# Optimization experiments

Measured on AMD Instinct MI355X. Metric: run time of the kernel, lower is better.

The kernel has to match this reference:

```python
import jax, jax.numpy as jnp
import numpy as np

HM = 256  # output_hm_shape


def _peak_grid(heatmap):
    # max_num_peaks=1 NMS -> global argmax per (b, joint) channel
    B, J, H, W = heatmap.shape
    idx = jnp.argmax(heatmap.reshape(B, J, H * W), axis=-1)
    y = (idx // W).astype(jnp.float32)
    x = (idx % W).astype(jnp.float32)
    ny = (H - 1) / 2.0
    nx = (W - 1) / 2.0
    # normalized (gx, gy) in [-1, 1], note (row,col) -> (x,y) flip as in source
    return jnp.stack([(x - nx) / nx, (y - ny) / ny], axis=-1)  # [B, J, 2]


def _bilinear_sample(feat, grid):
    # feat: [B, C, H, W], grid: [B, N, 2] (gx, gy), align_corners=True
    B, C, H, W = feat.shape
    x = (grid[..., 0] + 1.0) * 0.5 * (W - 1)
    y = (grid[..., 1] + 1.0) * 0.5 * (H - 1)
    x0 = jnp.floor(x); y0 = jnp.floor(y)
    wx = x - x0; wy = y - y0
    x0i = jnp.clip(x0, 0, W - 1).astype(jnp.int32)
    x1i = jnp.clip(x0 + 1, 0, W - 1).astype(jnp.int32)
    y0i = jnp.clip(y0, 0, H - 1).astype(jnp.int32)
    y1i = jnp.clip(y0 + 1, 0, H - 1).astype(jnp.int32)
    ff = feat.reshape(B, C, H * W)
    def g(iy, ix):
        return jnp.take_along_axis(ff, (iy * W + ix)[:, None, :], axis=2)  # [B, C, N]
    wx = wx[:, None, :]; wy = wy[:, None, :]
    return (g(y0i, x0i) * (1 - wx) * (1 - wy) + g(y0i, x1i) * wx * (1 - wy)
            + g(y1i, x0i) * (1 - wx) * wy + g(y1i, x1i) * wx * wy)


def _nearest_sample(feat, grid):
    B, C, H, W = feat.shape
    ix = jnp.clip(jnp.round((grid[..., 0] + 1.0) * 0.5 * (W - 1)), 0, W - 1).astype(jnp.int32)
    iy = jnp.clip(jnp.round((grid[..., 1] + 1.0) * 0.5 * (H - 1)), 0, H - 1).astype(jnp.int32)
    ff = feat.reshape(B, C, H * W)
    return jnp.take_along_axis(ff, (iy * W + ix)[:, None, :], axis=2)  # [B, C, N]


def _mlp(x, Ws, bs):
    # ReLU on every layer including last (is_activation_last=True)
    for W, b in zip(Ws, bs):
        x = jax.nn.relu(x @ W + b)
    return x


def setup_inputs() -> dict:
    key = jax.random.key(0)
    ks = jax.random.split(key, 16)
    inp = {
        'heatmap': jax.random.normal(ks[0], (16, 64, HM, HM), jnp.float32),
        'pos_embed': jax.random.normal(ks[1], (16, 32, HM, HM), jnp.float32),
        'feat1': jax.random.normal(ks[2], (16, 96, 128, 128), jnp.float32),
        'feat2': jax.random.normal(ks[3], (16, 384, 64, 64), jnp.float32),
        'feat3': jax.random.normal(ks[4], (16, 512, 32, 32), jnp.float32),
    }
    dims = [992, 1024, 512, 256, 224]
    for i in range(4):
        fan = dims[i]
        inp[f'W{i+1}'] = jax.random.normal(ks[5 + i], (dims[i], dims[i + 1]), jnp.float32) / np.sqrt(fan)
        inp[f'b{i+1}'] = jnp.zeros((dims[i + 1],), jnp.float32)
    return inp


def reference(heatmap, pos_embed, feat1, feat2, feat3, W1, b1, W2, b2, W3, b3, W4, b4):
    grid = _peak_grid(heatmap)  # [B, J, 2], detached in original (cpu numpy)
    positions = _nearest_sample(pos_embed, grid)  # [B, 32, J]
    ms = jnp.concatenate([_bilinear_sample(feat1, grid),
                          _bilinear_sample(feat2, grid),
                          _bilinear_sample(feat3, grid)], axis=1)  # [B, 992, J]
    seq = _mlp(ms.transpose(0, 2, 1), [W1, W2, W3, W4], [b1, b2, b3, b4])  # [B, J, 224]
    input_seq = jnp.concatenate([seq.transpose(0, 2, 1), positions], axis=1)  # [B, 256, J]
    return input_seq
```

## Files before the change

kernel.cpp:

```cpp
#include <hip/hip_runtime.h>
#include <hip/hip_bf16.h>
#include <cstddef>
#include <cstdint>


typedef __attribute__((ext_vector_type(8))) short bf16x8;
typedef __attribute__((ext_vector_type(4))) float f32x4;

__global__ __launch_bounds__(256) void argmax_kernel(const float* __restrict__ hm,
                                                     int* __restrict__ peaks) {
    __shared__ float sval[256];
    __shared__ int   sidx[256];
    const int plane = blockIdx.x;
    const float4* p4 = (const float4*)(hm + (size_t)plane * 65536);
    const int tid = threadIdx.x;
    float best = -3.402823466e38f;
    int bidx = 0;
    for (int i = tid; i < 16384; i += 256) {
        float4 v = p4[i];
        int base = i << 2;
        if (v.x > best) { best = v.x; bidx = base; }
        if (v.y > best) { best = v.y; bidx = base + 1; }
        if (v.z > best) { best = v.z; bidx = base + 2; }
        if (v.w > best) { best = v.w; bidx = base + 3; }
    }
    sval[tid] = best; sidx[tid] = bidx;
    __syncthreads();
    for (int s = 128; s > 0; s >>= 1) {
        if (tid < s) {
            float ov = sval[tid + s]; int oi = sidx[tid + s];
            if (ov > sval[tid] || (ov == sval[tid] && oi < sidx[tid])) {
                sval[tid] = ov; sidx[tid] = oi;
            }
        }
        __syncthreads();
    }
    if (tid == 0) peaks[plane] = sidx[0];
}

__device__ inline void bilinear_block(const float* __restrict__ fb, int C, int H, int W,
                                      float gx, float gy,
                                      __hip_bfloat16* __restrict__ dst, int tid) {
    const float x = (gx + 1.0f) * 0.5f * (float)(W - 1);
    const float y = (gy + 1.0f) * 0.5f * (float)(H - 1);
    const float x0f = floorf(x), y0f = floorf(y);
    const float wx = x - x0f, wy = y - y0f;
    const int x0 = (int)fminf(fmaxf(x0f,       0.f), (float)(W - 1));
    const int x1 = (int)fminf(fmaxf(x0f + 1.f, 0.f), (float)(W - 1));
    const int y0 = (int)fminf(fmaxf(y0f,       0.f), (float)(H - 1));
    const int y1 = (int)fminf(fmaxf(y0f + 1.f, 0.f), (float)(H - 1));
    const float w00 = (1.f - wx) * (1.f - wy);
    const float w01 = wx * (1.f - wy);
    const float w10 = (1.f - wx) * wy;
    const float w11 = wx * wy;
    const int i00 = y0 * W + x0, i01 = y0 * W + x1;
    const int i10 = y1 * W + x0, i11 = y1 * W + x1;
    const size_t HW = (size_t)H * W;
    for (int c = tid; c < C; c += 256) {
        const float* fc = fb + (size_t)c * HW;
        float v = fc[i00] * w00 + fc[i01] * w01 + fc[i10] * w10 + fc[i11] * w11;
        dst[c] = __float2bfloat16(v);
    }
}

__global__ __launch_bounds__(256) void gather_kernel(
    const float* __restrict__ pos_embed,
    const float* __restrict__ feat1, const float* __restrict__ feat2,
    const float* __restrict__ feat3,
    const int* __restrict__ peaks,
    __hip_bfloat16* __restrict__ X0, float* __restrict__ out) {
    const int plane = blockIdx.x;
    const int b = plane >> 6, j = plane & 63;
    const int idx = peaks[plane];
    const int py = idx >> 8, px = idx & 255;
    const float gx = ((float)px - 127.5f) / 127.5f;
    const float gy = ((float)py - 127.5f) / 127.5f;
    const int tid = threadIdx.x;

    if (tid < 32) {
        float v = pos_embed[((size_t)(b * 32 + tid)) * 65536 + idx];
        out[(size_t)b * 16384 + (size_t)(224 + tid) * 64 + j] = v;
    }

    __hip_bfloat16* xrow = X0 + (size_t)plane * 992;
    bilinear_block(feat1 + (size_t)b *  96 * 128 * 128,  96, 128, 128, gx, gy, xrow,       tid);
    bilinear_block(feat2 + (size_t)b * 384 *  64 *  64, 384,  64,  64, gx, gy, xrow +  96, tid);
    bilinear_block(feat3 + (size_t)b * 512 *  32 *  32, 512,  32,  32, gx, gy, xrow + 480, tid);
}

__global__ __launch_bounds__(256) void wcast_kernel(
    const float* __restrict__ W1, const float* __restrict__ W2,
    const float* __restrict__ W3, const float* __restrict__ W4,
    __hip_bfloat16* __restrict__ T1, __hip_bfloat16* __restrict__ T2,
    __hip_bfloat16* __restrict__ T3, __hip_bfloat16* __restrict__ T4) {
    int bid = blockIdx.x;
    const float* W; __hip_bfloat16* T; int K, N;
    if (bid < 992)        { W = W1; T = T1; K = 992;  N = 1024; }
    else if (bid < 1504)  { bid -= 992;  W = W2; T = T2; K = 1024; N = 512; }
    else if (bid < 1632)  { bid -= 1504; W = W3; T = T3; K = 512;  N = 256; }
    else                  { bid -= 1632; W = W4; T = T4; K = 256;  N = 224; }
    const int tilesN = N >> 5;
    const int tk = bid / tilesN, tn = bid - tk * tilesN;
    __shared__ float tile[32][33];
    const int col = threadIdx.x & 31, rowg = threadIdx.x >> 5;
    #pragma unroll
    for (int i = 0; i < 4; ++i) {
        int k = (tk << 5) + rowg + (i << 3);
        tile[rowg + (i << 3)][col] = W[(size_t)k * N + (tn << 5) + col];
    }
    __syncthreads();
    #pragma unroll
    for (int i = 0; i < 4; ++i) {
        int n = (tn << 5) + rowg + (i << 3);
        T[(size_t)n * K + (tk << 5) + col] = __float2bfloat16(tile[col][rowg + (i << 3)]);
    }
}

template<bool LAST>
__global__ __launch_bounds__(64) void mfma_gemm(
    const short* __restrict__ A, const short* __restrict__ Bt,
    const float* __restrict__ bias, void* __restrict__ Yv,
    int N, int K) {
    const int lane = threadIdx.x;
    const int q = lane >> 4, r = lane & 15;
    const int m0 = blockIdx.y << 5;
    const int n0 = blockIdx.x << 5;

    const short* pa0 = A  + (size_t)(m0 + r) * K + (q << 3);
    const short* pa1 = pa0 + (size_t)16 * K;
    const short* pb0 = Bt + (size_t)(n0 + r) * K + (q << 3);
    const short* pb1 = pb0 + (size_t)16 * K;

    f32x4 acc00 = {0.f,0.f,0.f,0.f}, acc01 = {0.f,0.f,0.f,0.f};
    f32x4 acc10 = {0.f,0.f,0.f,0.f}, acc11 = {0.f,0.f,0.f,0.f};

    bf16x8 a0 = *(const bf16x8*)pa0;
    bf16x8 a1 = *(const bf16x8*)pa1;
    bf16x8 b0 = *(const bf16x8*)pb0;
    bf16x8 b1 = *(const bf16x8*)pb1;

    for (int k = 32; k < K; k += 32) {
        bf16x8 na0 = *(const bf16x8*)(pa0 + k);
        bf16x8 na1 = *(const bf16x8*)(pa1 + k);
        bf16x8 nb0 = *(const bf16x8*)(pb0 + k);
        bf16x8 nb1 = *(const bf16x8*)(pb1 + k);
        acc00 = __builtin_amdgcn_mfma_f32_16x16x32_bf16(a0, b0, acc00, 0, 0, 0);
        acc01 = __builtin_amdgcn_mfma_f32_16x16x32_bf16(a0, b1, acc01, 0, 0, 0);
        acc10 = __builtin_amdgcn_mfma_f32_16x16x32_bf16(a1, b0, acc10, 0, 0, 0);
        acc11 = __builtin_amdgcn_mfma_f32_16x16x32_bf16(a1, b1, acc11, 0, 0, 0);
        a0 = na0; a1 = na1; b0 = nb0; b1 = nb1;
    }
    acc00 = __builtin_amdgcn_mfma_f32_16x16x32_bf16(a0, b0, acc00, 0, 0, 0);
    acc01 = __builtin_amdgcn_mfma_f32_16x16x32_bf16(a0, b1, acc01, 0, 0, 0);
    acc10 = __builtin_amdgcn_mfma_f32_16x16x32_bf16(a1, b0, acc10, 0, 0, 0);
    acc11 = __builtin_amdgcn_mfma_f32_16x16x32_bf16(a1, b1, acc11, 0, 0, 0);

    const float bias0 = bias[n0 + r];
    const float bias1 = bias[n0 + 16 + r];
    #pragma unroll
    for (int i = 0; i < 4; ++i) {
        const int row0 = m0 + (q << 2) + i;
        const int row1 = row0 + 16;
        float v00 = fmaxf(acc00[i] + bias0, 0.f);
        float v01 = fmaxf(acc01[i] + bias1, 0.f);
        float v10 = fmaxf(acc10[i] + bias0, 0.f);
        float v11 = fmaxf(acc11[i] + bias1, 0.f);
        if (LAST) {
            float* O = (float*)Yv;
            const int b0r = row0 >> 6, j0 = row0 & 63;
            const int b1r = row1 >> 6, j1 = row1 & 63;
            O[(size_t)b0r * 16384 + (size_t)(n0 + r)      * 64 + j0] = v00;
            O[(size_t)b0r * 16384 + (size_t)(n0 + 16 + r) * 64 + j0] = v01;
            O[(size_t)b1r * 16384 + (size_t)(n0 + r)      * 64 + j1] = v10;
            O[(size_t)b1r * 16384 + (size_t)(n0 + 16 + r) * 64 + j1] = v11;
        } else {
            __hip_bfloat16* Y = (__hip_bfloat16*)Yv;
            Y[(size_t)row0 * N + n0 + r]      = __float2bfloat16(v00);
            Y[(size_t)row0 * N + n0 + 16 + r] = __float2bfloat16(v01);
            Y[(size_t)row1 * N + n0 + r]      = __float2bfloat16(v10);
            Y[(size_t)row1 * N + n0 + 16 + r] = __float2bfloat16(v11);
        }
    }
}

extern "C" void kernel_launch(void* const* d_in, const int* in_sizes, int n_in,
                              void* d_out, int out_size, void* d_ws, size_t ws_size,
                              hipStream_t stream) {
    (void)in_sizes; (void)n_in; (void)out_size; (void)ws_size;
    const float* heatmap   = (const float*)d_in[0];
    const float* pos_embed = (const float*)d_in[1];
    const float* feat1     = (const float*)d_in[2];
    const float* feat2     = (const float*)d_in[3];
    const float* feat3     = (const float*)d_in[4];
    const float* W1 = (const float*)d_in[5];  const float* b1 = (const float*)d_in[6];
    const float* W2 = (const float*)d_in[7];  const float* b2 = (const float*)d_in[8];
    const float* W3 = (const float*)d_in[9];  const float* b3 = (const float*)d_in[10];
    const float* W4 = (const float*)d_in[11]; const float* b4 = (const float*)d_in[12];
    float* out = (float*)d_out;

    char* ws = (char*)d_ws;
    int*   peaks = (int*)ws;
    short* X0 = (short*)(ws + 8192);
    short* X1 = X0 + (size_t)1024 * 992;
    short* X2 = X1 + (size_t)1024 * 1024;
    short* X3 = X2 + (size_t)1024 * 512;
    short* T1 = X3 + (size_t)1024 * 256;
    short* T2 = T1 + (size_t)1024 * 992;
    short* T3 = T2 + (size_t)512 * 1024;
    short* T4 = T3 + (size_t)256 * 512;

    wcast_kernel<<<1688, 256, 0, stream>>>(W1, W2, W3, W4,
        (__hip_bfloat16*)T1, (__hip_bfloat16*)T2, (__hip_bfloat16*)T3, (__hip_bfloat16*)T4);
    argmax_kernel<<<1024, 256, 0, stream>>>(heatmap, peaks);
    gather_kernel<<<1024, 256, 0, stream>>>(pos_embed, feat1, feat2, feat3, peaks,
                                            (__hip_bfloat16*)X0, out);
    mfma_gemm<false><<<dim3(32, 32), 64, 0, stream>>>(X0, T1, b1, X1, 1024,  992);
    mfma_gemm<false><<<dim3(16, 32), 64, 0, stream>>>(X1, T2, b2, X2,  512, 1024);
    mfma_gemm<false><<<dim3( 8, 32), 64, 0, stream>>>(X2, T3, b3, X3,  256,  512);
    mfma_gemm<true ><<<dim3( 7, 32), 64, 0, stream>>>(X3, T4, b4, out, 224,  256);
}
```

Measured before the change: 604.4 us.

## Fuse argmax, gather and weight cast into a single front kernel

Merges the argmax, feature-gather and weight transpose/cast kernels into one launch. Blocks 0-1023 compute the per-plane argmax and then gather directly from the shared-memory result, so the peaks round trip through global memory goes away. Blocks 1024 and up perform the weight cast. This removes two kernel launches and their serialization, and lets the weight cast overlap with the heatmap scan. The cost is a shared-memory footprint sized for the larger of the two roles, and a heterogeneous grid.

```diff
diff --git a/kernel.cpp b/kernel.cpp
--- a/kernel.cpp
+++ b/kernel.cpp
@@ -6,37 +6,6 @@
 
 typedef __attribute__((ext_vector_type(8))) short bf16x8;
 typedef __attribute__((ext_vector_type(4))) float f32x4;
-
-__global__ __launch_bounds__(256) void argmax_kernel(const float* __restrict__ hm,
-                                                     int* __restrict__ peaks) {
-    __shared__ float sval[256];
-    __shared__ int   sidx[256];
-    const int plane = blockIdx.x;
-    const float4* p4 = (const float4*)(hm + (size_t)plane * 65536);
-    const int tid = threadIdx.x;
-    float best = -3.402823466e38f;
-    int bidx = 0;
-    for (int i = tid; i < 16384; i += 256) {
-        float4 v = p4[i];
-        int base = i << 2;
-        if (v.x > best) { best = v.x; bidx = base; }
-        if (v.y > best) { best = v.y; bidx = base + 1; }
-        if (v.z > best) { best = v.z; bidx = base + 2; }
-        if (v.w > best) { best = v.w; bidx = base + 3; }
-    }
-    sval[tid] = best; sidx[tid] = bidx;
-    __syncthreads();
-    for (int s = 128; s > 0; s >>= 1) {
-        if (tid < s) {
-            float ov = sval[tid + s]; int oi = sidx[tid + s];
-            if (ov > sval[tid] || (ov == sval[tid] && oi < sidx[tid])) {
-                sval[tid] = ov; sidx[tid] = oi;
-            }
-        }
-        __syncthreads();
-    }
-    if (tid == 0) peaks[plane] = sidx[0];
-}
 
 __device__ inline void bilinear_block(const float* __restrict__ fb, int C, int H, int W,
                                       float gx, float gy,
@@ -63,19 +32,75 @@
     }
 }
 
-__global__ __launch_bounds__(256) void gather_kernel(
+__global__ __launch_bounds__(256) void fused_front_kernel(
+    const float* __restrict__ hm,
     const float* __restrict__ pos_embed,
     const float* __restrict__ feat1, const float* __restrict__ feat2,
     const float* __restrict__ feat3,
-    const int* __restrict__ peaks,
+    const float* __restrict__ W1, const float* __restrict__ W2,
+    const float* __restrict__ W3, const float* __restrict__ W4,
+    __hip_bfloat16* __restrict__ T1, __hip_bfloat16* __restrict__ T2,
+    __hip_bfloat16* __restrict__ T3, __hip_bfloat16* __restrict__ T4,
     __hip_bfloat16* __restrict__ X0, float* __restrict__ out) {
+    __shared__ float smem[32 * 33];
+    float* sval = smem;
+    int*   sidx = (int*)(smem + 256);
+    const int tid = threadIdx.x;
+
+    if (blockIdx.x >= 1024) {
+        int bid = blockIdx.x - 1024;
+        const float* W; __hip_bfloat16* T; int K, N;
+        if (bid < 992)        { W = W1; T = T1; K = 992;  N = 1024; }
+        else if (bid < 1504)  { bid -= 992;  W = W2; T = T2; K = 1024; N = 512; }
+        else if (bid < 1632)  { bid -= 1504; W = W3; T = T3; K = 512;  N = 256; }
+        else                  { bid -= 1632; W = W4; T = T4; K = 256;  N = 224; }
+        const int tilesN = N >> 5;
+        const int tk = bid / tilesN, tn = bid - tk * tilesN;
+        float (*tile)[33] = (float(*)[33])smem;
+        const int col = tid & 31, rowg = tid >> 5;
+        #pragma unroll
+        for (int i = 0; i < 4; ++i) {
+            int k = (tk << 5) + rowg + (i << 3);
+            tile[rowg + (i << 3)][col] = W[(size_t)k * N + (tn << 5) + col];
+        }
+        __syncthreads();
+        #pragma unroll
+        for (int i = 0; i < 4; ++i) {
+            int n = (tn << 5) + rowg + (i << 3);
+            T[(size_t)n * K + (tk << 5) + col] = __float2bfloat16(tile[col][rowg + (i << 3)]);
+        }
+        return;
+    }
+
     const int plane = blockIdx.x;
+    const float4* p4 = (const float4*)(hm + (size_t)plane * 65536);
+    float best = -3.402823466e38f;
+    int bidx = 0;
+    for (int i = tid; i < 16384; i += 256) {
+        float4 v = p4[i];
+        int base = i << 2;
+        if (v.x > best) { best = v.x; bidx = base; }
+        if (v.y > best) { best = v.y; bidx = base + 1; }
+        if (v.z > best) { best = v.z; bidx = base + 2; }
+        if (v.w > best) { best = v.w; bidx = base + 3; }
+    }
+    sval[tid] = best; sidx[tid] = bidx;
+    __syncthreads();
+    for (int s = 128; s > 0; s >>= 1) {
+        if (tid < s) {
+            float ov = sval[tid + s]; int oi = sidx[tid + s];
+            if (ov > sval[tid] || (ov == sval[tid] && oi < sidx[tid])) {
+                sval[tid] = ov; sidx[tid] = oi;
+            }
+        }
+        __syncthreads();
+    }
+    const int idx = sidx[0];
+
     const int b = plane >> 6, j = plane & 63;
-    const int idx = peaks[plane];
     const int py = idx >> 8, px = idx & 255;
     const float gx = ((float)px - 127.5f) / 127.5f;
     const float gy = ((float)py - 127.5f) / 127.5f;
-    const int tid = threadIdx.x;
 
     if (tid < 32) {
         float v = pos_embed[((size_t)(b * 32 + tid)) * 65536 + idx];
@@ -86,34 +111,6 @@
     bilinear_block(feat1 + (size_t)b *  96 * 128 * 128,  96, 128, 128, gx, gy, xrow,       tid);
     bilinear_block(feat2 + (size_t)b * 384 *  64 *  64, 384,  64,  64, gx, gy, xrow +  96, tid);
     bilinear_block(feat3 + (size_t)b * 512 *  32 *  32, 512,  32,  32, gx, gy, xrow + 480, tid);
-}
-
-__global__ __launch_bounds__(256) void wcast_kernel(
-    const float* __restrict__ W1, const float* __restrict__ W2,
-    const float* __restrict__ W3, const float* __restrict__ W4,
-    __hip_bfloat16* __restrict__ T1, __hip_bfloat16* __restrict__ T2,
-    __hip_bfloat16* __restrict__ T3, __hip_bfloat16* __restrict__ T4) {
-    int bid = blockIdx.x;
-    const float* W; __hip_bfloat16* T; int K, N;
-    if (bid < 992)        { W = W1; T = T1; K = 992;  N = 1024; }
-    else if (bid < 1504)  { bid -= 992;  W = W2; T = T2; K = 1024; N = 512; }
-    else if (bid < 1632)  { bid -= 1504; W = W3; T = T3; K = 512;  N = 256; }
-    else                  { bid -= 1632; W = W4; T = T4; K = 256;  N = 224; }
-    const int tilesN = N >> 5;
-    const int tk = bid / tilesN, tn = bid - tk * tilesN;
-    __shared__ float tile[32][33];
-    const int col = threadIdx.x & 31, rowg = threadIdx.x >> 5;
-    #pragma unroll
-    for (int i = 0; i < 4; ++i) {
-        int k = (tk << 5) + rowg + (i << 3);
-        tile[rowg + (i << 3)][col] = W[(size_t)k * N + (tn << 5) + col];
-    }
-    __syncthreads();
-    #pragma unroll
-    for (int i = 0; i < 4; ++i) {
-        int n = (tn << 5) + rowg + (i << 3);
-        T[(size_t)n * K + (tk << 5) + col] = __float2bfloat16(tile[col][rowg + (i << 3)]);
-    }
 }
 
 template<bool LAST>
@@ -199,7 +196,6 @@
     float* out = (float*)d_out;
 
     char* ws = (char*)d_ws;
-    int*   peaks = (int*)ws;
     short* X0 = (short*)(ws + 8192);
     short* X1 = X0 + (size_t)1024 * 992;
     short* X2 = X1 + (size_t)1024 * 1024;
@@ -209,11 +205,11 @@
     short* T3 = T2 + (size_t)512 * 1024;
     short* T4 = T3 + (size_t)256 * 512;
 
-    wcast_kernel<<<1688, 256, 0, stream>>>(W1, W2, W3, W4,
-        (__hip_bfloat16*)T1, (__hip_bfloat16*)T2, (__hip_bfloat16*)T3, (__hip_bfloat16*)T4);
-    argmax_kernel<<<1024, 256, 0, stream>>>(heatmap, peaks);
-    gather_kernel<<<1024, 256, 0, stream>>>(pos_embed, feat1, feat2, feat3, peaks,
-                                            (__hip_bfloat16*)X0, out);
+    fused_front_kernel<<<2712, 256, 0, stream>>>(
+        heatmap, pos_embed, feat1, feat2, feat3,
+        W1, W2, W3, W4,
+        (__hip_bfloat16*)T1, (__hip_bfloat16*)T2, (__hip_bfloat16*)T3, (__hip_bfloat16*)T4,
+        (__hip_bfloat16*)X0, out);
     mfma_gemm<false><<<dim3(32, 32), 64, 0, stream>>>(X0, T1, b1, X1, 1024,  992);
     mfma_gemm<false><<<dim3(16, 32), 64, 0, stream>>>(X1, T2, b2, X2,  512, 1024);
     mfma_gemm<false><<<dim3( 8, 32), 64, 0, stream>>>(X2, T3, b3, X3,  256,  512);
```

Measured after the change: 596.0 us. About the same (-1.4%).
